# Optimization experiments

Hardware: AMD Instinct MI355X
Metric: run time of the kernel (lower is better)

## Reference

```python
import jax, jax.numpy as jnp
import numpy as np

N = 50000   # nodes
E = 800000  # edges
D = 128     # hidden_dim
LN_EPS = 1e-5


def _mlp2(x, W1, b1, W2, b2, act_last):
    y = jax.nn.silu(x @ W1 + b1)
    y = y @ W2 + b2
    return jax.nn.silu(y) if act_last else y


def setup_inputs() -> dict:
    key = jax.random.key(0)
    ks = jax.random.split(key, 20)
    s = 1.0 / np.sqrt(D)
    inp = {
        "h": jax.random.normal(ks[0], (N, D), jnp.float32),
        "x": jax.random.normal(ks[1], (N, 3), jnp.float32),
        "vel_all": jax.random.normal(ks[2], (N, 5, 3), jnp.float32),
        "edge_index": jax.random.randint(ks[3], (2, E), 0, N, jnp.int64),
        # phi_e: Linear(2D+11, D) -> SiLU -> Linear(D, D) -> SiLU   (weights stored [in,out])
        "We1": jax.random.uniform(ks[4], (2 * D + 11, D), jnp.float32, -s, s),
        "be1": jax.random.uniform(ks[5], (D,), jnp.float32, -s, s),
        "We2": jax.random.uniform(ks[6], (D, D), jnp.float32, -s, s),
        "be2": jax.random.uniform(ks[7], (D,), jnp.float32, -s, s),
        # phi_x: Linear(D, D) -> SiLU -> Linear(D, 1)
        "Wx1": jax.random.uniform(ks[8], (D, D), jnp.float32, -s, s),
        "bx1": jax.random.uniform(ks[9], (D,), jnp.float32, -s, s),
        "Wx2": jax.random.uniform(ks[10], (D, 1), jnp.float32, -s, s),
        "bx2": jax.random.uniform(ks[11], (1,), jnp.float32, -s, s),
        # phi_h: Linear(2D, D) -> SiLU -> Linear(D, D)
        "Wh1": jax.random.uniform(ks[12], (2 * D, D), jnp.float32, -s, s),
        "bh1": jax.random.uniform(ks[13], (D,), jnp.float32, -s, s),
        "Wh2": jax.random.uniform(ks[14], (D, D), jnp.float32, -s, s),
        "bh2": jax.random.uniform(ks[15], (D,), jnp.float32, -s, s),
        # LayerNorm(D)
        "gamma": jnp.ones((D,), jnp.float32),
        "beta": jnp.zeros((D,), jnp.float32),
    }
    return inp


def reference(h, x, vel_all, edge_index, We1, be1, We2, be2, Wx1, bx1, Wx2, bx2,
              Wh1, bh1, Wh2, bh2, gamma, beta):
    n = h.shape[0]
    src, dst = edge_index[0], edge_index[1]

    rel = x[src] - x[dst]                                  # [E,3]
    dist2 = jnp.sum(rel * rel, axis=-1, keepdims=True)     # [E,1]
    dist = jnp.maximum(jnp.sqrt(dist2), 1e-8)
    r_hat = rel / dist                                     # [E,3]

    vel_proj_src = jnp.sum(vel_all[src] * r_hat[:, None, :], axis=-1)  # [E,5]
    vel_proj_dst = jnp.sum(vel_all[dst] * r_hat[:, None, :], axis=-1)  # [E,5]

    feat = jnp.concatenate([h[src], h[dst], dist2, vel_proj_src, vel_proj_dst], axis=-1)
    m_ij = _mlp2(feat, We1, be1, We2, be2, act_last=True)  # [E,D]

    # update_coords=True: scatter_mean of rel * phi_x(m_ij)
    coord_w = _mlp2(m_ij, Wx1, bx1, Wx2, bx2, act_last=False)          # [E,1]
    num = jax.ops.segment_sum(rel * coord_w, dst, num_segments=n)      # [N,3]
    cnt = jax.ops.segment_sum(jnp.ones((rel.shape[0], 1), x.dtype), dst, num_segments=n)
    delta_x = num / jnp.maximum(cnt, 1.0)
    x = x + delta_x

    agg = jax.ops.segment_sum(m_ij, dst, num_segments=n)               # [N,D]
    dh = _mlp2(jnp.concatenate([h, agg], axis=-1), Wh1, bh1, Wh2, bh2, act_last=False)
    h = h + dh  # dropout=0 -> identity

    # LayerNorm
    mu = jnp.mean(h, axis=-1, keepdims=True)
    var = jnp.mean(jnp.square(h - mu), axis=-1, keepdims=True)
    h = (h - mu) * jax.lax.rsqrt(var + LN_EPS) * gamma + beta

    return (h, x, m_ij)
```

## Files before the change

### kernel.cpp

```cpp
#include <hip/hip_runtime.h>
#include <stdint.h>

#define CAPB 64

typedef __attribute__((ext_vector_type(8))) short bf16x8;
typedef __attribute__((ext_vector_type(4))) float f32x4;

__device__ __forceinline__ float bf2f(unsigned short u){
  union { unsigned int i; float f; } v; v.i = ((unsigned int)u) << 16; return v.f;
}
__device__ __forceinline__ unsigned short f2bf(float f){
  union { float f; unsigned int i; } v; v.f = f;
  unsigned int x = v.i;
  unsigned int r = (x + 0x7FFFu + ((x >> 16) & 1u)) >> 16;
  return (unsigned short)r;
}
__device__ __forceinline__ float silu_f(float v){
  return v / (1.0f + __expf(-v));
}

template<bool F32> __device__ __forceinline__ float ldv(const void* p, size_t i){
  if (F32) return ((const float*)p)[i];
  return bf2f(((const unsigned short*)p)[i]);
}
template<bool F32> __device__ __forceinline__ void stv(void* p, size_t i, float v){
  if (F32) ((float*)p)[i] = v;
  else     ((unsigned short*)p)[i] = f2bf(v);
}
template<bool I64> __device__ __forceinline__ int ldidx(const int* p, size_t i){
  return I64 ? p[2*i] : p[i];
}

__global__ void detect_kernel(const unsigned int* gw, const int* eidx, int N, int* flags){
  int f = 0;
  if (gw[0] == 0x3F800000u) f |= 1;
  bool i64 = true;
  for (int k = 0; k < 4; k++){
    int lo = eidx[2*k], hi = eidx[2*k+1];
    if (hi != 0 || lo < 0 || lo >= N) i64 = false;
  }
  if (i64) f |= 2;
  flags[0] = f;
}

__global__ __launch_bounds__(256) void hist_kernel(
    const int* eidx, int* cnt_i, int* bucket, int* slot, int N, int E, const int* flags)
{
  int e = blockIdx.x * 256 + threadIdx.x;
  if (e >= E) return;
  int d;
  if (flags[0] & 2) d = eidx[2*((size_t)E + e)];
  else              d = eidx[(size_t)E + e];
  d = min(max(d, 0), N-1);
  int p = atomicAdd(&cnt_i[d], 1);
  slot[e] = p;
  if (p < CAPB) bucket[(size_t)d*CAPB + p] = e;
}

struct __align__(16) NodePreSmem { float hlt[128][36]; };

template<bool F32>
__device__ void node_pre_impl(NodePreSmem& S, const void* h, const void* We1,
                              unsigned short* H1a, unsigned short* H1b, int N)
{
  const int t = threadIdx.x;
  const int base = blockIdx.x * 32;
  for (int i = t; i < 32*128; i += 256){
    int nl = i >> 7, j = i & 127;
    int node = base + nl;
    S.hlt[j][nl] = (node < N) ? ldv<F32>(h, (size_t)node*128 + j) : 0.0f;
  }
  __syncthreads();
  const int j = t & 127, half = t >> 7;
  const size_t wbase = (size_t)(half * 128) * 128;
  unsigned short* O = half ? H1b : H1a;
  float acc[32];
  #pragma unroll
  for (int nl=0; nl<32; nl++) acc[nl] = 0.0f;
  for (int k=0; k<128; k++){
    float w = ldv<F32>(We1, wbase + (size_t)k*128 + j);
    const float4* row = (const float4*)&S.hlt[k][0];
    #pragma unroll
    for (int g=0; g<8; g++){
      float4 hv = row[g];
      acc[g*4+0] += hv.x * w;
      acc[g*4+1] += hv.y * w;
      acc[g*4+2] += hv.z * w;
      acc[g*4+3] += hv.w * w;
    }
  }
  #pragma unroll
  for (int nl=0; nl<32; nl++){
    int node = base + nl;
    if (node < N) O[(size_t)node*128 + j] = f2bf(acc[nl]);
  }
}

__global__ __launch_bounds__(256) void node_pre(
    const void* h, const void* We1, unsigned short* H1a, unsigned short* H1b,
    int N, const int* flags)
{
  __shared__ NodePreSmem S;
  if (flags[0] & 1) node_pre_impl<true >(S, h, We1, H1a, H1b, N);
  else              node_pre_impl<false>(S, h, We1, H1a, H1b, N);
}

struct __align__(16) EdgeSmem {
  unsigned short m1s[64][136];
  unsigned short m2s[64][136];
  float rels[64][3];
  float geos[64][11];
  int   dsts[64];
  int   srcs[64];
  int   slot[64];
  float wpart[4][64];
};

template<bool F32, bool I64>
__device__ void edge_impl(EdgeSmem& S,
    const void* xu, const void* velu, const int* eidx,
    const unsigned short* __restrict__ H1a, const unsigned short* __restrict__ H1b,
    const void* We1, const void* be1, const void* We2, const void* be2,
    const void* Wx1, const void* bx1, const void* Wx2, const void* bx2,
    void* out, size_t moff,
    float* __restrict__ agg, float* __restrict__ num,
    const int* __restrict__ slotp,
    int N, int E, int ntiles)
{
  const int t = threadIdx.x;
  const int wave = t >> 6, lane = t & 63;
  const int col = lane & 15, quad = lane >> 4;
  const int colbase = wave * 32;

  bf16x8 bwe2[2][4], bwx1[2][4];
  float wx2v[2], be2v[2], bx1v[2];
  #pragma unroll
  for (int nt=0; nt<2; nt++){
    int n = colbase + nt*16 + col;
    wx2v[nt] = ldv<F32>(Wx2, n);
    be2v[nt] = ldv<F32>(be2, n);
    bx1v[nt] = ldv<F32>(bx1, n);
    #pragma unroll
    for (int kb=0; kb<4; kb++){
      bf16x8 a, b;
      #pragma unroll
      for (int jj=0; jj<8; jj++){
        int k = kb*32 + quad*8 + jj;
        a[jj] = (short)f2bf(ldv<F32>(We2, (size_t)k*128 + n));
        b[jj] = (short)f2bf(ldv<F32>(Wx1, (size_t)k*128 + n));
      }
      bwe2[nt][kb] = a; bwx1[nt][kb] = b;
    }
  }
  const int j0 = 2*lane, j1 = 2*lane + 1;
  float gw0[11], gw1[11];
  #pragma unroll
  for (int k=0; k<11; k++){
    gw0[k] = ldv<F32>(We1, (size_t)(256+k)*128 + j0);
    gw1[k] = ldv<F32>(We1, (size_t)(256+k)*128 + j1);
  }
  const float be10 = ldv<F32>(be1, j0);
  const float be11 = ldv<F32>(be1, j1);
  const int jfix = t & 127;
  const float bx2v = ldv<F32>(bx2, 0);

  for (int tile = blockIdx.x; tile < ntiles; tile += gridDim.x){
    const int ebase = tile * 64;
    {
      const int el = t >> 2, part = t & 3;
      const int e = ebase + el;
      int s = 0, d = 0;
      if (e < E){ s = ldidx<I64>(eidx, e); d = ldidx<I64>(eidx, (size_t)E + e); }
      s = min(max(s, 0), N-1);
      d = min(max(d, 0), N-1);
      float rx = ldv<F32>(xu, (size_t)s*3+0) - ldv<F32>(xu, (size_t)d*3+0);
      float ry = ldv<F32>(xu, (size_t)s*3+1) - ldv<F32>(xu, (size_t)d*3+1);
      float rz = ldv<F32>(xu, (size_t)s*3+2) - ldv<F32>(xu, (size_t)d*3+2);
      float dist2 = rx*rx + ry*ry + rz*rz;
      float dist = fmaxf(sqrtf(dist2), 1e-8f);
      float inv = 1.0f / dist;
      float ux = rx*inv, uy = ry*inv, uz = rz*inv;
      if (part == 0){
        S.srcs[el] = s; S.dsts[el] = d;
        S.slot[el] = (e < E) ? slotp[e] : 0;
        S.rels[el][0]=rx; S.rels[el][1]=ry; S.rels[el][2]=rz;
        S.geos[el][0] = dist2;
      }
      for (int v = part; v < 10; v += 4){
        size_t bidx = (v < 5) ? ((size_t)s*15 + v*3) : ((size_t)d*15 + (v-5)*3);
        float pr = ldv<F32>(velu, bidx+0)*ux + ldv<F32>(velu, bidx+1)*uy + ldv<F32>(velu, bidx+2)*uz;
        S.geos[el][1+v] = pr;
      }
    }
    __syncthreads();
    #pragma unroll
    for (int it=0; it<16; it++){
      const int el = it*4 + wave;
      const int s = S.srcs[el], d = S.dsts[el];
      const unsigned int ua = *(const unsigned int*)&H1a[(size_t)s*128 + j0];
      const unsigned int ub = *(const unsigned int*)&H1b[(size_t)d*128 + j0];
      float a0 = bf2f((unsigned short)(ua & 0xFFFFu)) + bf2f((unsigned short)(ub & 0xFFFFu)) + be10;
      float a1 = bf2f((unsigned short)(ua >> 16))     + bf2f((unsigned short)(ub >> 16))     + be11;
      #pragma unroll
      for (int k=0; k<11; k++){
        float g = S.geos[el][k];
        a0 += gw0[k] * g;
        a1 += gw1[k] * g;
      }
      unsigned int pk = (unsigned int)f2bf(silu_f(a0)) | ((unsigned int)f2bf(silu_f(a1)) << 16);
      *(unsigned int*)&S.m1s[el][j0] = pk;
    }
    __syncthreads();
    #pragma unroll
    for (int et=0; et<4; et++){
      #pragma unroll
      for (int nt=0; nt<2; nt++){
        f32x4 acc = { be2v[nt], be2v[nt], be2v[nt], be2v[nt] };
        #pragma unroll
        for (int kb=0; kb<4; kb++){
          bf16x8 a = *(const bf16x8*)&S.m1s[et*16 + col][kb*32 + quad*8];
          acc = __builtin_amdgcn_mfma_f32_16x16x32_bf16(a, bwe2[nt][kb], acc, 0, 0, 0);
        }
        int n = colbase + nt*16 + col;
        #pragma unroll
        for (int r=0; r<4; r++)
          S.m2s[et*16 + quad*4 + r][n] = f2bf(silu_f(acc[r]));
      }
    }
    __syncthreads();
    if (F32){
      #pragma unroll
      for (int it=0; it<4; it++){
        const int sl = t + it*256;
        const int el = sl >> 4, i8 = sl & 15;
        const int e = ebase + el;
        if (e < E){
          const bf16x8 mv = *(const bf16x8*)&S.m2s[el][i8*8];
          float f[8];
          #pragma unroll
          for (int j=0; j<8; j++) f[j] = bf2f((unsigned short)mv[j]);
          float* op = (float*)out + moff + (size_t)e*128 + i8*8;
          float4 v0 = { f[0], f[1], f[2], f[3] };
          float4 v1 = { f[4], f[5], f[6], f[7] };
          *(float4*)op = v0;
          *(float4*)(op + 4) = v1;
          if (S.slot[el] >= CAPB){
            float* ap = &agg[(size_t)S.dsts[el]*128 + i8*8];
            #pragma unroll
            for (int j=0; j<8; j++) atomicAdd(ap + j, f[j]);
          }
        }
      }
    } else {
      #pragma unroll
      for (int it=0; it<32; it++){
        int el = (t + it*256) >> 7;
        int e = ebase + el;
        if (e < E){
          float v = bf2f(S.m2s[el][jfix]);
          stv<F32>(out, moff + (size_t)e*128 + jfix, v);
          atomicAdd(&agg[(size_t)S.dsts[el]*128 + jfix], v);
        }
      }
    }
    float part[4][4];
    #pragma unroll
    for (int et=0; et<4; et++)
      #pragma unroll
      for (int r=0; r<4; r++) part[et][r] = 0.0f;
    #pragma unroll
    for (int et=0; et<4; et++){
      #pragma unroll
      for (int nt=0; nt<2; nt++){
        f32x4 acc = { bx1v[nt], bx1v[nt], bx1v[nt], bx1v[nt] };
        #pragma unroll
        for (int kb=0; kb<4; kb++){
          bf16x8 a = *(const bf16x8*)&S.m2s[et*16 + col][kb*32 + quad*8];
          acc = __builtin_amdgcn_mfma_f32_16x16x32_bf16(a, bwx1[nt][kb], acc, 0, 0, 0);
        }
        #pragma unroll
        for (int r=0; r<4; r++) part[et][r] += silu_f(acc[r]) * wx2v[nt];
      }
    }
    #pragma unroll
    for (int et=0; et<4; et++){
      #pragma unroll
      for (int r=0; r<4; r++){
        float v = part[et][r];
        v += __shfl_xor(v, 1, 16);
        v += __shfl_xor(v, 2, 16);
        v += __shfl_xor(v, 4, 16);
        v += __shfl_xor(v, 8, 16);
        part[et][r] = v;
      }
    }
    if (col == 0){
      #pragma unroll
      for (int et=0; et<4; et++)
        #pragma unroll
        for (int r=0; r<4; r++)
          S.wpart[wave][et*16 + quad*4 + r] = part[et][r];
    }
    __syncthreads();
    if (t < 64){
      int e = ebase + t;
      if (e < E){
        float w = S.wpart[0][t] + S.wpart[1][t] + S.wpart[2][t] + S.wpart[3][t] + bx2v;
        int d = S.dsts[t];
        atomicAdd(&num[(size_t)d*3+0], S.rels[t][0]*w);
        atomicAdd(&num[(size_t)d*3+1], S.rels[t][1]*w);
        atomicAdd(&num[(size_t)d*3+2], S.rels[t][2]*w);
      }
    }
    __syncthreads();
  }
}

__global__ __launch_bounds__(256) void edge_kernel(
    const void* xu, const void* velu, const int* eidx,
    const unsigned short* H1a, const unsigned short* H1b,
    const void* We1, const void* be1, const void* We2, const void* be2,
    const void* Wx1, const void* bx1, const void* Wx2, const void* bx2,
    void* out, size_t moff, float* agg, float* num, const int* slotp,
    int N, int E, int ntiles, const int* flags)
{
  __shared__ EdgeSmem S;
  int f = flags[0];
  if      (f == 0) edge_impl<false,false>(S, xu, velu, eidx, H1a, H1b, We1, be1, We2, be2, Wx1, bx1, Wx2, bx2, out, moff, agg, num, slotp, N, E, ntiles);
  else if (f == 1) edge_impl<true ,false>(S, xu, velu, eidx, H1a, H1b, We1, be1, We2, be2, Wx1, bx1, Wx2, bx2, out, moff, agg, num, slotp, N, E, ntiles);
  else if (f == 2) edge_impl<false,true >(S, xu, velu, eidx, H1a, H1b, We1, be1, We2, be2, Wx1, bx1, Wx2, bx2, out, moff, agg, num, slotp, N, E, ntiles);
  else             edge_impl<true ,true >(S, xu, velu, eidx, H1a, H1b, We1, be1, We2, be2, Wx1, bx1, Wx2, bx2, out, moff, agg, num, slotp, N, E, ntiles);
}

struct __align__(16) NodeFinalSmem {
  unsigned short ins[16][256];
  unsigned short y1s[16][128];
  float hns[16][128];
};

template<bool F32>
__device__ void node_final_impl(NodeFinalSmem& S,
    const void* h, const void* xu,
    const float* __restrict__ agg, const float* __restrict__ num,
    const int* __restrict__ cnt_i, const int* __restrict__ bucket,
    const void* Wh1, const void* bh1, const void* Wh2, const void* bh2,
    const void* gam, const void* bet,
    void* out, size_t xoff, size_t moff, int N)
{
  const int t = threadIdx.x;
  const int base = blockIdx.x * 16;
  for (int i = t; i < 16*128; i += 256){
    int n = i >> 7, c = i & 127;
    int node = base + n;
    S.ins[n][c] = (node < N) ? f2bf(ldv<F32>(h, (size_t)node*128 + c)) : (unsigned short)0;
  }
  if (F32){
    const int g = t >> 4, i8 = t & 15;
    const int node = base + g;
    float a[8] = {0,0,0,0,0,0,0,0};
    if (node < N){
      int deg = cnt_i[node];
      int kmax = min(deg, CAPB);
      const float* mbase = (const float*)out + moff;
      for (int k = 0; k < kmax; k++){
        int e = bucket[(size_t)node*CAPB + k];
        const float* rp = mbase + (size_t)e*128 + i8*8;
        float4 v0 = *(const float4*)rp;
        float4 v1 = *(const float4*)(rp + 4);
        a[0]+=v0.x; a[1]+=v0.y; a[2]+=v0.z; a[3]+=v0.w;
        a[4]+=v1.x; a[5]+=v1.y; a[6]+=v1.z; a[7]+=v1.w;
      }
      if (deg > CAPB){
        const float* ap = &agg[(size_t)node*128 + i8*8];
        #pragma unroll
        for (int j=0; j<8; j++) a[j] += ap[j];
      }
    }
    #pragma unroll
    for (int j=0; j<8; j++) S.ins[g][128 + i8*8 + j] = f2bf(a[j]);
  } else {
    for (int i = t; i < 16*128; i += 256){
      int n = i >> 7, c = i & 127;
      int node = base + n;
      S.ins[n][128 + c] = (node < N) ? f2bf(agg[(size_t)node*128 + c]) : (unsigned short)0;
    }
  }
  __syncthreads();
  const int j = t & 127, nh = t >> 7;
  {
    float acc[8];
    #pragma unroll
    for (int u=0; u<8; u++) acc[u] = ldv<F32>(bh1, j);
    for (int k=0; k<256; k++){
      float w = ldv<F32>(Wh1, (size_t)k*128 + j);
      #pragma unroll
      for (int u=0; u<8; u++) acc[u] += bf2f(S.ins[nh + 2*u][k]) * w;
    }
    #pragma unroll
    for (int u=0; u<8; u++) S.y1s[nh + 2*u][j] = f2bf(silu_f(acc[u]));
  }
  __syncthreads();
  {
    float acc[8];
    #pragma unroll
    for (int u=0; u<8; u++) acc[u] = ldv<F32>(bh2, j);
    for (int k=0; k<128; k++){
      float w = ldv<F32>(Wh2, (size_t)k*128 + j);
      #pragma unroll
      for (int u=0; u<8; u++) acc[u] += bf2f(S.y1s[nh + 2*u][k]) * w;
    }
    #pragma unroll
    for (int u=0; u<8; u++){
      int n = nh + 2*u;
      int node = base + n;
      float hv = (node < N) ? ldv<F32>(h, (size_t)node*128 + j) : 0.0f;
      S.hns[n][j] = hv + acc[u];
    }
  }
  __syncthreads();
  {
    int n = t >> 4, sub = t & 15;
    float s = 0.0f, ss = 0.0f;
    #pragma unroll
    for (int i2=0; i2<8; i2++){
      float v = S.hns[n][sub + 16*i2];
      s += v; ss += v*v;
    }
    #pragma unroll
    for (int m=1; m<16; m<<=1){ s += __shfl_xor(s, m, 16); ss += __shfl_xor(ss, m, 16); }
    float mu = s * (1.0f/128.0f);
    float var = fmaxf(ss * (1.0f/128.0f) - mu*mu, 0.0f);
    float rs = rsqrtf(var + 1e-5f);
    int gnode = base + n;
    if (gnode < N){
      #pragma unroll
      for (int i2=0; i2<8; i2++){
        int jj = sub + 16*i2;
        float v = (S.hns[n][jj] - mu) * rs * ldv<F32>(gam, jj) + ldv<F32>(bet, jj);
        stv<F32>(out, (size_t)gnode*128 + jj, v);
      }
    }
  }
  if (t < 48){
    int n = t / 3, c = t % 3;
    int node = base + n;
    if (node < N){
      float cv = fmaxf((float)cnt_i[node], 1.0f);
      float dx = num[(size_t)node*3 + c] / cv;
      stv<F32>(out, xoff + (size_t)node*3 + c, ldv<F32>(xu, (size_t)node*3 + c) + dx);
    }
  }
}

__global__ __launch_bounds__(256) void node_final(
    const void* h, const void* xu,
    const float* agg, const float* num, const int* cnt_i, const int* bucket,
    const void* Wh1, const void* bh1, const void* Wh2, const void* bh2,
    const void* gam, const void* bet,
    void* out, size_t xoff, size_t moff, int N, const int* flags)
{
  __shared__ NodeFinalSmem S;
  if (flags[0] & 1) node_final_impl<true >(S, h, xu, agg, num, cnt_i, bucket, Wh1, bh1, Wh2, bh2, gam, bet, out, xoff, moff, N);
  else              node_final_impl<false>(S, h, xu, agg, num, cnt_i, bucket, Wh1, bh1, Wh2, bh2, gam, bet, out, xoff, moff, N);
}

extern "C" void kernel_launch(void* const* d_in, const int* in_sizes, int n_in,
                              void* d_out, int out_size, void* d_ws, size_t ws_size,
                              hipStream_t stream)
{
  const int N = in_sizes[0] / 128;
  const int E = in_sizes[3] / 2;

  char* ws = (char*)d_ws;
  int* flags = (int*)ws;
  unsigned short* H1a = (unsigned short*)(ws + 256);
  unsigned short* H1b = H1a + (size_t)N * 128;
  float* agg   = (float*)(ws + 256 + (size_t)N * 128 * 2 * 2);
  float* num   = agg + (size_t)N * 128;
  int*   cnt_i = (int*)(num + (size_t)N * 3);
  int*   bucket = cnt_i + N;
  int*   slot   = bucket + (size_t)N * CAPB;

  detect_kernel<<<1, 1, 0, stream>>>((const unsigned int*)d_in[16], (const int*)d_in[3], N, flags);

  size_t zbytes = ((size_t)N*128 + (size_t)N*3 + (size_t)N) * 4;
  hipMemsetAsync((void*)agg, 0, zbytes, stream);

  hist_kernel<<<(E + 255) / 256, 256, 0, stream>>>((const int*)d_in[3], cnt_i, bucket, slot, N, E, flags);

  node_pre<<<(N + 31) / 32, 256, 0, stream>>>(d_in[0], d_in[4], H1a, H1b, N, flags);

  size_t xoff = (size_t)N * 128;
  size_t moff = (size_t)N * 128 + (size_t)N * 3;
  int ntiles = (E + 63) / 64;
  edge_kernel<<<2500, 256, 0, stream>>>(d_in[1], d_in[2], (const int*)d_in[3], H1a, H1b,
                                        d_in[4], d_in[5], d_in[6], d_in[7],
                                        d_in[8], d_in[9], d_in[10], d_in[11],
                                        d_out, moff, agg, num, slot, N, E, ntiles, flags);

  node_final<<<(N + 15) / 16, 256, 0, stream>>>(d_in[0], d_in[1], agg, num, cnt_i, bucket,
                                                d_in[12], d_in[13], d_in[14], d_in[15],
                                                d_in[16], d_in[17],
                                                d_out, xoff, moff, N, flags);
}
```

Measured before the change: 1.502 ms.

## Split edge kernel into separate first-layer gather kernel and MFMA GEMM kernel

Splits the fused edge kernel in two. The first kernel computes the first-layer activations (the gathered H1 sums plus the geometric features, then SiLU) for each edge with a lane-parallel layout and writes them to workspace, or into the m_ij output slot when the workspace is too small. The second kernel reads them back in tiles for the MFMA layers and scatters. This is meant to remove the gather latency and the extra syncs from the MFMA kernel, at the cost of an extra E×128 write and read through global memory. It also broadcasts bucket indices with shuffles in the node aggregation and adds unroll pragmas to the node GEMM loops.

```diff
diff --git a/kernel.cpp b/kernel.cpp
--- a/kernel.cpp
+++ b/kernel.cpp
@@ -77,6 +77,7 @@
   float acc[32];
   #pragma unroll
   for (int nl=0; nl<32; nl++) acc[nl] = 0.0f;
+  #pragma unroll 2
   for (int k=0; k<128; k++){
     float w = ldv<F32>(We1, wbase + (size_t)k*128 + j);
     const float4* row = (const float4*)&S.hlt[k][0];
@@ -105,23 +106,113 @@
   else              node_pre_impl<false>(S, h, We1, H1a, H1b, N);
 }
 
-struct __align__(16) EdgeSmem {
+template<bool F32, bool I64, bool M1F32>
+__device__ void m1_impl(
+    const void* xu, const void* velu, const int* eidx,
+    const unsigned short* __restrict__ H1a, const unsigned short* __restrict__ H1b,
+    const void* We1, const void* be1,
+    void* m1p, int N, int E)
+{
+  const int t = threadIdx.x;
+  const int sub = t & 31;
+  const int j0 = sub * 4;
+  float gw[11][4];
+  #pragma unroll
+  for (int k=0;k<11;k++)
+    #pragma unroll
+    for (int c=0;c<4;c++) gw[k][c] = ldv<F32>(We1, (size_t)(256+k)*128 + j0 + c);
+  float b1[4];
+  #pragma unroll
+  for (int c=0;c<4;c++) b1[c] = ldv<F32>(be1, j0 + c);
+
+  int gid = blockIdx.x * 8 + (t >> 5);
+  const int gstride = gridDim.x * 8;
+  for (int e = gid; e < E; e += gstride){
+    int s = ldidx<I64>(eidx, e);
+    int d = ldidx<I64>(eidx, (size_t)E + e);
+    s = min(max(s, 0), N-1);
+    d = min(max(d, 0), N-1);
+    float rx = ldv<F32>(xu,(size_t)s*3+0) - ldv<F32>(xu,(size_t)d*3+0);
+    float ry = ldv<F32>(xu,(size_t)s*3+1) - ldv<F32>(xu,(size_t)d*3+1);
+    float rz = ldv<F32>(xu,(size_t)s*3+2) - ldv<F32>(xu,(size_t)d*3+2);
+    float dist2 = rx*rx + ry*ry + rz*rz;
+    float dist = fmaxf(sqrtf(dist2), 1e-8f);
+    float inv = 1.0f / dist;
+    float ux = rx*inv, uy = ry*inv, uz = rz*inv;
+    float geo[11];
+    geo[0] = dist2;
+    #pragma unroll
+    for (int v=0; v<5; v++){
+      geo[1+v] = ldv<F32>(velu,(size_t)s*15+v*3+0)*ux + ldv<F32>(velu,(size_t)s*15+v*3+1)*uy + ldv<F32>(velu,(size_t)s*15+v*3+2)*uz;
+      geo[6+v] = ldv<F32>(velu,(size_t)d*15+v*3+0)*ux + ldv<F32>(velu,(size_t)d*15+v*3+1)*uy + ldv<F32>(velu,(size_t)d*15+v*3+2)*uz;
+    }
+    uint2 ua = *(const uint2*)&H1a[(size_t)s*128 + j0];
+    uint2 ub = *(const uint2*)&H1b[(size_t)d*128 + j0];
+    float a[4];
+    a[0] = bf2f((unsigned short)(ua.x & 0xFFFFu)) + bf2f((unsigned short)(ub.x & 0xFFFFu)) + b1[0];
+    a[1] = bf2f((unsigned short)(ua.x >> 16))     + bf2f((unsigned short)(ub.x >> 16))     + b1[1];
+    a[2] = bf2f((unsigned short)(ua.y & 0xFFFFu)) + bf2f((unsigned short)(ub.y & 0xFFFFu)) + b1[2];
+    a[3] = bf2f((unsigned short)(ua.y >> 16))     + bf2f((unsigned short)(ub.y >> 16))     + b1[3];
+    #pragma unroll
+    for (int k=0;k<11;k++){
+      float g = geo[k];
+      #pragma unroll
+      for (int c=0;c<4;c++) a[c] += gw[k][c] * g;
+    }
+    #pragma unroll
+    for (int c=0;c<4;c++) a[c] = silu_f(a[c]);
+    if (M1F32){
+      float4 v = { a[0], a[1], a[2], a[3] };
+      *(float4*)((float*)m1p + (size_t)e*128 + j0) = v;
+    } else {
+      uint2 p;
+      p.x = (unsigned int)f2bf(a[0]) | ((unsigned int)f2bf(a[1]) << 16);
+      p.y = (unsigned int)f2bf(a[2]) | ((unsigned int)f2bf(a[3]) << 16);
+      *(uint2*)((unsigned short*)m1p + (size_t)e*128 + j0) = p;
+    }
+  }
+}
+
+template<bool USE_WS>
+__global__ __launch_bounds__(256) void m1_kernel(
+    const void* xu, const void* velu, const int* eidx,
+    const unsigned short* H1a, const unsigned short* H1b,
+    const void* We1, const void* be1,
+    void* m1ws, void* out, size_t moff, int N, int E, const int* flags)
+{
+  int f = flags[0];
+  if (USE_WS){
+    if      (f == 0) m1_impl<false,false,false>(xu,velu,eidx,H1a,H1b,We1,be1,m1ws,N,E);
+    else if (f == 1) m1_impl<true ,false,false>(xu,velu,eidx,H1a,H1b,We1,be1,m1ws,N,E);
+    else if (f == 2) m1_impl<false,true ,false>(xu,velu,eidx,H1a,H1b,We1,be1,m1ws,N,E);
+    else             m1_impl<true ,true ,false>(xu,velu,eidx,H1a,H1b,We1,be1,m1ws,N,E);
+  } else {
+    if (f & 1){
+      void* p = (void*)((float*)out + moff);
+      if (f & 2) m1_impl<true,true ,true>(xu,velu,eidx,H1a,H1b,We1,be1,p,N,E);
+      else       m1_impl<true,false,true>(xu,velu,eidx,H1a,H1b,We1,be1,p,N,E);
+    } else {
+      void* p = (void*)((unsigned short*)out + moff);
+      if (f & 2) m1_impl<false,true ,false>(xu,velu,eidx,H1a,H1b,We1,be1,p,N,E);
+      else       m1_impl<false,false,false>(xu,velu,eidx,H1a,H1b,We1,be1,p,N,E);
+    }
+  }
+}
+
+struct __align__(16) GemmSmem {
   unsigned short m1s[64][136];
   unsigned short m2s[64][136];
-  float rels[64][3];
-  float geos[64][11];
+  float relv[192];
   int   dsts[64];
-  int   srcs[64];
   int   slot[64];
   float wpart[4][64];
 };
 
-template<bool F32, bool I64>
-__device__ void edge_impl(EdgeSmem& S,
-    const void* xu, const void* velu, const int* eidx,
-    const unsigned short* __restrict__ H1a, const unsigned short* __restrict__ H1b,
-    const void* We1, const void* be1, const void* We2, const void* be2,
-    const void* Wx1, const void* bx1, const void* Wx2, const void* bx2,
+template<bool F32, bool I64, bool M1F32>
+__device__ void gemm_impl(GemmSmem& S,
+    const void* xu, const int* eidx, const void* m1p,
+    const void* We2, const void* be2, const void* Wx1, const void* bx1,
+    const void* Wx2, const void* bx2,
     void* out, size_t moff,
     float* __restrict__ agg, float* __restrict__ num,
     const int* __restrict__ slotp,
@@ -152,63 +243,48 @@
       bwe2[nt][kb] = a; bwx1[nt][kb] = b;
     }
   }
-  const int j0 = 2*lane, j1 = 2*lane + 1;
-  float gw0[11], gw1[11];
-  #pragma unroll
-  for (int k=0; k<11; k++){
-    gw0[k] = ldv<F32>(We1, (size_t)(256+k)*128 + j0);
-    gw1[k] = ldv<F32>(We1, (size_t)(256+k)*128 + j1);
-  }
-  const float be10 = ldv<F32>(be1, j0);
-  const float be11 = ldv<F32>(be1, j1);
   const int jfix = t & 127;
   const float bx2v = ldv<F32>(bx2, 0);
+  const int srow = t >> 2, sseg = t & 3;
 
   for (int tile = blockIdx.x; tile < ntiles; tile += gridDim.x){
     const int ebase = tile * 64;
     {
-      const int el = t >> 2, part = t & 3;
-      const int e = ebase + el;
-      int s = 0, d = 0;
-      if (e < E){ s = ldidx<I64>(eidx, e); d = ldidx<I64>(eidx, (size_t)E + e); }
-      s = min(max(s, 0), N-1);
-      d = min(max(d, 0), N-1);
-      float rx = ldv<F32>(xu, (size_t)s*3+0) - ldv<F32>(xu, (size_t)d*3+0);
-      float ry = ldv<F32>(xu, (size_t)s*3+1) - ldv<F32>(xu, (size_t)d*3+1);
-      float rz = ldv<F32>(xu, (size_t)s*3+2) - ldv<F32>(xu, (size_t)d*3+2);
-      float dist2 = rx*rx + ry*ry + rz*rz;
-      float dist = fmaxf(sqrtf(dist2), 1e-8f);
-      float inv = 1.0f / dist;
-      float ux = rx*inv, uy = ry*inv, uz = rz*inv;
-      if (part == 0){
-        S.srcs[el] = s; S.dsts[el] = d;
-        S.slot[el] = (e < E) ? slotp[e] : 0;
-        S.rels[el][0]=rx; S.rels[el][1]=ry; S.rels[el][2]=rz;
-        S.geos[el][0] = dist2;
-      }
-      for (int v = part; v < 10; v += 4){
-        size_t bidx = (v < 5) ? ((size_t)s*15 + v*3) : ((size_t)d*15 + (v-5)*3);
-        float pr = ldv<F32>(velu, bidx+0)*ux + ldv<F32>(velu, bidx+1)*uy + ldv<F32>(velu, bidx+2)*uz;
-        S.geos[el][1+v] = pr;
-      }
-    }
-    __syncthreads();
-    #pragma unroll
-    for (int it=0; it<16; it++){
-      const int el = it*4 + wave;
-      const int s = S.srcs[el], d = S.dsts[el];
-      const unsigned int ua = *(const unsigned int*)&H1a[(size_t)s*128 + j0];
-      const unsigned int ub = *(const unsigned int*)&H1b[(size_t)d*128 + j0];
-      float a0 = bf2f((unsigned short)(ua & 0xFFFFu)) + bf2f((unsigned short)(ub & 0xFFFFu)) + be10;
-      float a1 = bf2f((unsigned short)(ua >> 16))     + bf2f((unsigned short)(ub >> 16))     + be11;
-      #pragma unroll
-      for (int k=0; k<11; k++){
-        float g = S.geos[el][k];
-        a0 += gw0[k] * g;
-        a1 += gw1[k] * g;
-      }
-      unsigned int pk = (unsigned int)f2bf(silu_f(a0)) | ((unsigned int)f2bf(silu_f(a1)) << 16);
-      *(unsigned int*)&S.m1s[el][j0] = pk;
+      const int e = ebase + srow;
+      if (M1F32){
+        const float* rp = (const float*)m1p + (size_t)e*128 + sseg*32;
+        #pragma unroll
+        for (int q=0;q<4;q++){
+          float4 va = {0,0,0,0}, vb = {0,0,0,0};
+          if (e < E){ va = *(const float4*)(rp + q*8); vb = *(const float4*)(rp + q*8 + 4); }
+          bf16x8 w;
+          w[0]=(short)f2bf(va.x); w[1]=(short)f2bf(va.y); w[2]=(short)f2bf(va.z); w[3]=(short)f2bf(va.w);
+          w[4]=(short)f2bf(vb.x); w[5]=(short)f2bf(vb.y); w[6]=(short)f2bf(vb.z); w[7]=(short)f2bf(vb.w);
+          *(bf16x8*)&S.m1s[srow][sseg*32 + q*8] = w;
+        }
+      } else {
+        const unsigned short* rp = (const unsigned short*)m1p + (size_t)e*128 + sseg*32;
+        #pragma unroll
+        for (int q=0;q<4;q++){
+          bf16x8 w = {0,0,0,0,0,0,0,0};
+          if (e < E) w = *(const bf16x8*)(rp + q*8);
+          *(bf16x8*)&S.m1s[srow][sseg*32 + q*8] = w;
+        }
+      }
+      if (t < 64){
+        int e2 = ebase + t;
+        int s2 = 0, d2 = 0, sl = 0;
+        if (e2 < E){
+          s2 = ldidx<I64>(eidx, e2);
+          d2 = ldidx<I64>(eidx, (size_t)E + e2);
+          sl = slotp[e2];
+        }
+        s2 = min(max(s2,0), N-1); d2 = min(max(d2,0), N-1);
+        S.dsts[t] = d2; S.slot[t] = sl;
+        S.relv[t*3+0] = ldv<F32>(xu,(size_t)s2*3+0) - ldv<F32>(xu,(size_t)d2*3+0);
+        S.relv[t*3+1] = ldv<F32>(xu,(size_t)s2*3+1) - ldv<F32>(xu,(size_t)d2*3+1);
+        S.relv[t*3+2] = ldv<F32>(xu,(size_t)s2*3+2) - ldv<F32>(xu,(size_t)d2*3+2);
+      }
     }
     __syncthreads();
     #pragma unroll
@@ -307,29 +383,41 @@
       if (e < E){
         float w = S.wpart[0][t] + S.wpart[1][t] + S.wpart[2][t] + S.wpart[3][t] + bx2v;
         int d = S.dsts[t];
-        atomicAdd(&num[(size_t)d*3+0], S.rels[t][0]*w);
-        atomicAdd(&num[(size_t)d*3+1], S.rels[t][1]*w);
-        atomicAdd(&num[(size_t)d*3+2], S.rels[t][2]*w);
+        atomicAdd(&num[(size_t)d*3+0], S.relv[t*3+0]*w);
+        atomicAdd(&num[(size_t)d*3+1], S.relv[t*3+1]*w);
+        atomicAdd(&num[(size_t)d*3+2], S.relv[t*3+2]*w);
       }
     }
     __syncthreads();
   }
 }
 
-__global__ __launch_bounds__(256) void edge_kernel(
-    const void* xu, const void* velu, const int* eidx,
-    const unsigned short* H1a, const unsigned short* H1b,
-    const void* We1, const void* be1, const void* We2, const void* be2,
-    const void* Wx1, const void* bx1, const void* Wx2, const void* bx2,
+template<bool USE_WS>
+__global__ __launch_bounds__(256) void gemm_kernel(
+    const void* xu, const int* eidx, const void* m1ws,
+    const void* We2, const void* be2, const void* Wx1, const void* bx1,
+    const void* Wx2, const void* bx2,
     void* out, size_t moff, float* agg, float* num, const int* slotp,
     int N, int E, int ntiles, const int* flags)
 {
-  __shared__ EdgeSmem S;
+  __shared__ GemmSmem S;
   int f = flags[0];
-  if      (f == 0) edge_impl<false,false>(S, xu, velu, eidx, H1a, H1b, We1, be1, We2, be2, Wx1, bx1, Wx2, bx2, out, moff, agg, num, slotp, N, E, ntiles);
-  else if (f == 1) edge_impl<true ,false>(S, xu, velu, eidx, H1a, H1b, We1, be1, We2, be2, Wx1, bx1, Wx2, bx2, out, moff, agg, num, slotp, N, E, ntiles);
-  else if (f == 2) edge_impl<false,true >(S, xu, velu, eidx, H1a, H1b, We1, be1, We2, be2, Wx1, bx1, Wx2, bx2, out, moff, agg, num, slotp, N, E, ntiles);
-  else             edge_impl<true ,true >(S, xu, velu, eidx, H1a, H1b, We1, be1, We2, be2, Wx1, bx1, Wx2, bx2, out, moff, agg, num, slotp, N, E, ntiles);
+  if (USE_WS){
+    if      (f == 0) gemm_impl<false,false,false>(S, xu, eidx, m1ws, We2,be2,Wx1,bx1,Wx2,bx2, out,moff, agg,num, slotp, N,E,ntiles);
+    else if (f == 1) gemm_impl<true ,false,false>(S, xu, eidx, m1ws, We2,be2,Wx1,bx1,Wx2,bx2, out,moff, agg,num, slotp, N,E,ntiles);
+    else if (f == 2) gemm_impl<false,true ,false>(S, xu, eidx, m1ws, We2,be2,Wx1,bx1,Wx2,bx2, out,moff, agg,num, slotp, N,E,ntiles);
+    else             gemm_impl<true ,true ,false>(S, xu, eidx, m1ws, We2,be2,Wx1,bx1,Wx2,bx2, out,moff, agg,num, slotp, N,E,ntiles);
+  } else {
+    if (f & 1){
+      const void* p = (const void*)((float*)out + moff);
+      if (f & 2) gemm_impl<true,true ,true>(S, xu, eidx, p, We2,be2,Wx1,bx1,Wx2,bx2, out,moff, agg,num, slotp, N,E,ntiles);
+      else       gemm_impl<true,false,true>(S, xu, eidx, p, We2,be2,Wx1,bx1,Wx2,bx2, out,moff, agg,num, slotp, N,E,ntiles);
+    } else {
+      const void* p = (const void*)((unsigned short*)out + moff);
+      if (f & 2) gemm_impl<false,true ,false>(S, xu, eidx, p, We2,be2,Wx1,bx1,Wx2,bx2, out,moff, agg,num, slotp, N,E,ntiles);
+      else       gemm_impl<false,false,false>(S, xu, eidx, p, We2,be2,Wx1,bx1,Wx2,bx2, out,moff, agg,num, slotp, N,E,ntiles);
+    }
+  }
 }
 
 struct __align__(16) NodeFinalSmem {
@@ -356,19 +444,28 @@
   }
   if (F32){
     const int g = t >> 4, i8 = t & 15;
+    const int lanebase = (t & 63) & ~15;
     const int node = base + g;
     float a[8] = {0,0,0,0,0,0,0,0};
     if (node < N){
       int deg = cnt_i[node];
       int kmax = min(deg, CAPB);
       const float* mbase = (const float*)out + moff;
-      for (int k = 0; k < kmax; k++){
-        int e = bucket[(size_t)node*CAPB + k];
-        const float* rp = mbase + (size_t)e*128 + i8*8;
-        float4 v0 = *(const float4*)rp;
-        float4 v1 = *(const float4*)(rp + 4);
-        a[0]+=v0.x; a[1]+=v0.y; a[2]+=v0.z; a[3]+=v0.w;
-        a[4]+=v1.x; a[5]+=v1.y; a[6]+=v1.z; a[7]+=v1.w;
+      for (int c0 = 0; c0 < kmax; c0 += 16){
+        int ee = 0;
+        if (c0 + i8 < kmax) ee = bucket[(size_t)node*CAPB + c0 + i8];
+        int cnum = min(16, kmax - c0);
+        #pragma unroll
+        for (int k = 0; k < 16; k++){
+          if (k < cnum){
+            int e = __shfl(ee, lanebase + k, 64);
+            const float* rp = mbase + (size_t)e*128 + i8*8;
+            float4 v0 = *(const float4*)rp;
+            float4 v1 = *(const float4*)(rp + 4);
+            a[0]+=v0.x; a[1]+=v0.y; a[2]+=v0.z; a[3]+=v0.w;
+            a[4]+=v1.x; a[5]+=v1.y; a[6]+=v1.z; a[7]+=v1.w;
+          }
+        }
       }
       if (deg > CAPB){
         const float* ap = &agg[(size_t)node*128 + i8*8];
@@ -391,6 +488,7 @@
     float acc[8];
     #pragma unroll
     for (int u=0; u<8; u++) acc[u] = ldv<F32>(bh1, j);
+    #pragma unroll 4
     for (int k=0; k<256; k++){
       float w = ldv<F32>(Wh1, (size_t)k*128 + j);
       #pragma unroll
@@ -404,6 +502,7 @@
     float acc[8];
     #pragma unroll
     for (int u=0; u<8; u++) acc[u] = ldv<F32>(bh2, j);
+    #pragma unroll 4
     for (int k=0; k<128; k++){
       float w = ldv<F32>(Wh2, (size_t)k*128 + j);
       #pragma unroll
@@ -473,17 +572,20 @@
 
   char* ws = (char*)d_ws;
   int* flags = (int*)ws;
-  unsigned short* H1a = (unsigned short*)(ws + 256);
-  unsigned short* H1b = H1a + (size_t)N * 128;
-  float* agg   = (float*)(ws + 256 + (size_t)N * 128 * 2 * 2);
-  float* num   = agg + (size_t)N * 128;
-  int*   cnt_i = (int*)(num + (size_t)N * 3);
-  int*   bucket = cnt_i + N;
-  int*   slot   = bucket + (size_t)N * CAPB;
+  size_t off = 256;
+  unsigned short* H1a = (unsigned short*)(ws + off); off += (size_t)N*256;
+  unsigned short* H1b = (unsigned short*)(ws + off); off += (size_t)N*256;
+  float* agg   = (float*)(ws + off); off += (size_t)N*512;
+  float* num   = (float*)(ws + off); off += (size_t)N*12;
+  int*   cnt_i = (int*)(ws + off); off += (size_t)N*4;
+  int*   bucket= (int*)(ws + off); off += (size_t)N*CAPB*4;
+  int*   slot  = (int*)(ws + off); off += (size_t)E*4;
+  void*  m1ws  = (void*)(ws + off); off += (size_t)E*256;
+  const bool use_ws = (off <= ws_size);
 
   detect_kernel<<<1, 1, 0, stream>>>((const unsigned int*)d_in[16], (const int*)d_in[3], N, flags);
 
-  size_t zbytes = ((size_t)N*128 + (size_t)N*3 + (size_t)N) * 4;
+  size_t zbytes = (size_t)N*512 + (size_t)N*12 + (size_t)N*4;
   hipMemsetAsync((void*)agg, 0, zbytes, stream);
 
   hist_kernel<<<(E + 255) / 256, 256, 0, stream>>>((const int*)d_in[3], cnt_i, bucket, slot, N, E, flags);
@@ -493,10 +595,22 @@
   size_t xoff = (size_t)N * 128;
   size_t moff = (size_t)N * 128 + (size_t)N * 3;
   int ntiles = (E + 63) / 64;
-  edge_kernel<<<2500, 256, 0, stream>>>(d_in[1], d_in[2], (const int*)d_in[3], H1a, H1b,
-                                        d_in[4], d_in[5], d_in[6], d_in[7],
-                                        d_in[8], d_in[9], d_in[10], d_in[11],
-                                        d_out, moff, agg, num, slot, N, E, ntiles, flags);
+
+  if (use_ws){
+    m1_kernel<true><<<2048, 256, 0, stream>>>(d_in[1], d_in[2], (const int*)d_in[3], H1a, H1b,
+                                              d_in[4], d_in[5], m1ws, d_out, moff, N, E, flags);
+    gemm_kernel<true><<<2500, 256, 0, stream>>>(d_in[1], (const int*)d_in[3], m1ws,
+                                                d_in[6], d_in[7], d_in[8], d_in[9],
+                                                d_in[10], d_in[11],
+                                                d_out, moff, agg, num, slot, N, E, ntiles, flags);
+  } else {
+    m1_kernel<false><<<2048, 256, 0, stream>>>(d_in[1], d_in[2], (const int*)d_in[3], H1a, H1b,
+                                               d_in[4], d_in[5], m1ws, d_out, moff, N, E, flags);
+    gemm_kernel<false><<<2500, 256, 0, stream>>>(d_in[1], (const int*)d_in[3], m1ws,
+                                                 d_in[6], d_in[7], d_in[8], d_in[9],
+                                                 d_in[10], d_in[11],
+                                                 d_out, moff, agg, num, slot, N, E, ntiles, flags);
+  }
 
   node_final<<<(N + 15) / 16, 256, 0, stream>>>(d_in[0], d_in[1], agg, num, cnt_i, bucket,
                                                 d_in[12], d_in[13], d_in[14], d_in[15],
```

New measurement: 1.311 ms. 12.7% less time.
